# Performance work log

Measured on AMD Instinct MI355X. Metric: run time of the kernel, lower is better.

The kernel has to match this reference:

```python
import jax, jax.numpy as jnp
import numpy as np

B, T, S, E, H = 2, 2048, 2048, 1024, 16
DH = E // H

def setup_inputs() -> dict:
    key = jax.random.key(0)
    ks = jax.random.split(key, 12)
    sc = 1.0 / np.sqrt(E)
    inp = {
        'query': jax.random.normal(ks[0], (B, T, E), jnp.float32),
        'key':   jax.random.normal(ks[1], (B, S, E), jnp.float32),
        'value': jax.random.normal(ks[2], (B, S, E), jnp.float32),
        'Wq': jax.random.normal(ks[3], (E, E), jnp.float32) * sc,
        'bq': jnp.zeros((E,), jnp.float32),
        'Wk': jax.random.normal(ks[4], (E, E), jnp.float32) * sc,
        'bk': jnp.zeros((E,), jnp.float32),
        'Wv': jax.random.normal(ks[5], (E, E), jnp.float32) * sc,
        'bv': jnp.zeros((E,), jnp.float32),
        'Wo': jax.random.normal(ks[6], (E, E), jnp.float32) * sc,
        'bo': jnp.zeros((E,), jnp.float32),
    }
    return inp

def reference(query, key, value, Wq, bq, Wk, bk, Wv, bv, Wo, bo):
    # Linear projections (torch nn.Linear: x @ W.T + b)
    Q = query @ Wq.T + bq          # [B,T,E]
    K = key   @ Wk.T + bk          # [B,S,E]
    V = value @ Wv.T + bv          # [B,S,E]
    # split heads -> [B,H,L,DH]
    Q = Q.reshape(B, T, H, DH).transpose(0, 2, 1, 3)
    K = K.reshape(B, S, H, DH).transpose(0, 2, 1, 3)
    V = V.reshape(B, S, H, DH).transpose(0, 2, 1, 3)
    scores = jnp.einsum('bhtd,bhsd->bhts', Q, K) / jnp.sqrt(jnp.float32(DH))
    attn = jax.nn.softmax(scores, axis=-1)            # [B,H,T,S]
    out = jnp.einsum('bhts,bhsd->bhtd', attn, V)      # [B,H,T,DH]
    out = out.transpose(0, 2, 1, 3).reshape(B, T, E)
    out = out @ Wo.T + bo                             # [B,T,E]
    attn_avg = attn.mean(axis=1)                      # average_attn_weights=True
    return out, attn_avg
```

## Files before the change

kernel.cpp:

```cpp
#include <hip/hip_runtime.h>

#define DEV __device__ __forceinline__

typedef __attribute__((ext_vector_type(8))) short short8;
typedef __attribute__((ext_vector_type(4))) float floatx4;
typedef __attribute__((ext_vector_type(2))) unsigned int uint2v;
typedef unsigned short u16;

DEV u16 f2bf(float f) {
  unsigned int u = __float_as_uint(f);
  u += 0x7fffu + ((u >> 16) & 1u);
  return (u16)(u >> 16);
}

DEV unsigned int cvtpk(float a, float b) {
  unsigned int r;
  asm("v_cvt_pk_bf16_f32 %0, %1, %2" : "=v"(r) : "v"(a), "v"(b));
  return r;
}

DEV void load16_to_lds(const void* g, void* l) {
  __builtin_amdgcn_global_load_lds(
      (const __attribute__((address_space(1))) unsigned int*)g,
      (__attribute__((address_space(3))) unsigned int*)l, 16, 0, 0);
}

DEV int xcd_swz(int flat, int nwg) {
  return (flat & 7) * (nwg >> 3) + (flat >> 3);
}

#define MFMA16(A, B, C) __builtin_amdgcn_mfma_f32_16x16x32_bf16(A, B, C, 0, 0, 0)
#define EXP2(x) __builtin_amdgcn_exp2f(x)

#define QSCALE 0.18033688011112042f

DEV void stage_block(const u16* src_row0, int k0, int ln, void* ldsbase) {
  int r = ln >> 2;
  int p = ((ln & 3) - (ln >> 4)) & 3;
  load16_to_lds((const char*)(src_row0 + (size_t)r * 1024 + k0) + p * 16, ldsbase);
}
DEV const short8* frag_addr(const u16* base, int blk, int c, int q) {
  int slot = c * 4 + ((q + (c >> 2)) & 3);
  return (const short8*)(base + blk * 512 + slot * 8);
}

__global__ __launch_bounds__(256) void cvt_all(
    const float* __restrict__ w0, const float* __restrict__ w1,
    const float* __restrict__ w2, const float* __restrict__ w3,
    const float* __restrict__ a0, const float* __restrict__ a1, const float* __restrict__ a2,
    u16* __restrict__ e0, u16* __restrict__ e1, u16* __restrict__ e2, u16* __restrict__ e3,
    u16* __restrict__ f0, u16* __restrict__ f1, u16* __restrict__ f2) {
  const int t = blockIdx.y;
  const float* s;
  u16* d;
  size_t base;
  if (t < 4) {
    s = t == 0 ? w0 : t == 1 ? w1 : t == 2 ? w2 : w3;
    d = t == 0 ? e0 : t == 1 ? e1 : t == 2 ? e2 : e3;
    base = 0;
  } else {
    int a = (t - 4) >> 2;
    s = a == 0 ? a0 : a == 1 ? a1 : a2;
    d = a == 0 ? f0 : a == 1 ? f1 : f2;
    base = (size_t)((t - 4) & 3) * 1048576;
  }
  size_t i = base + (size_t)(blockIdx.x * 256 + threadIdx.x) * 4;
  float4 v = *(const float4*)(s + i);
  ushort4 o;
  o.x = f2bf(v.x); o.y = f2bf(v.y); o.z = f2bf(v.z); o.w = f2bf(v.w);
  *(ushort4*)(d + i) = o;
}

__global__ __launch_bounds__(512, 4) void qkv_gemm(
    const u16* __restrict__ qb, const u16* __restrict__ kb, const u16* __restrict__ vb,
    const u16* __restrict__ wq, const u16* __restrict__ wk, const u16* __restrict__ wv,
    const float* __restrict__ bq, const float* __restrict__ bk, const float* __restrict__ bv,
    u16* __restrict__ Qh, u16* __restrict__ Kh, u16* __restrict__ VT) {
  __shared__ __align__(16) u16 As[2][8192];
  __shared__ __align__(16) u16 Bs[2][4096];
  const int tid = threadIdx.x;
  const int w = tid >> 6, ln = tid & 63, q = ln >> 4, c = ln & 15;
  const int wr = w >> 1, wc = w & 1;
  const int z = blockIdx.z;
  int m_idx, n_idx;
  if (z == 2) {
    int f2 = blockIdx.x + 8 * blockIdx.y;
    n_idx = f2 & 31;
    m_idx = f2 >> 5;
  } else {
    n_idx = blockIdx.x;
    m_idx = blockIdx.y;
  }
  const int m0 = m_idx * 256, n0 = n_idx * 128;
  const u16* Asrc = z == 0 ? qb : (z == 1 ? kb : wv);
  const u16* Bsrc = z == 0 ? wq : (z == 1 ? wk : vb);

  floatx4 acc[4][4];
#pragma unroll
  for (int i = 0; i < 4; ++i)
#pragma unroll
    for (int j = 0; j < 4; ++j) acc[i][j] = (floatx4){0.f, 0.f, 0.f, 0.f};

#pragma unroll
  for (int j = 0; j < 3; ++j) {
    int idx = w * 3 + j;
    if (idx < 16)
      stage_block(Asrc + (size_t)(m0 + idx * 16) * 1024, 0, ln, (char*)As[0] + idx * 1024);
    else
      stage_block(Bsrc + (size_t)(n0 + (idx - 16) * 16) * 1024, 0, ln, (char*)Bs[0] + (idx - 16) * 1024);
  }

  int cur = 0;
  for (int k0 = 0; k0 < 1024; k0 += 32) {
    __syncthreads();
    if (k0 + 32 < 1024) {
      const int nb = cur ^ 1;
#pragma unroll
      for (int j = 0; j < 3; ++j) {
        int idx = w * 3 + j;
        if (idx < 16)
          stage_block(Asrc + (size_t)(m0 + idx * 16) * 1024, k0 + 32, ln, (char*)As[nb] + idx * 1024);
        else
          stage_block(Bsrc + (size_t)(n0 + (idx - 16) * 16) * 1024, k0 + 32, ln,
                      (char*)Bs[nb] + (idx - 16) * 1024);
      }
    }
    short8 a[4], bb[4];
#pragma unroll
    for (int mt = 0; mt < 4; ++mt) a[mt] = *frag_addr(As[cur], wr * 4 + mt, c, q);
#pragma unroll
    for (int nt = 0; nt < 4; ++nt) bb[nt] = *frag_addr(Bs[cur], wc * 4 + nt, c, q);
    __builtin_amdgcn_s_setprio(1);
#pragma unroll
    for (int mt = 0; mt < 4; ++mt)
#pragma unroll
      for (int nt = 0; nt < 4; ++nt) acc[mt][nt] = MFMA16(a[mt], bb[nt], acc[mt][nt]);
    __builtin_amdgcn_s_setprio(0);
    cur ^= 1;
  }

  if (z <= 1) {
    const float* bias = z ? bk : bq;
    u16* dst = z ? Kh : Qh;
    const float scale = z ? 1.0f : QSCALE;
    float bn[4];
#pragma unroll
    for (int nt = 0; nt < 4; ++nt) bn[nt] = bias[n0 + wc * 64 + nt * 16 + c];
#pragma unroll
    for (int mt = 0; mt < 4; ++mt)
#pragma unroll
      for (int r = 0; r < 4; ++r) {
        int m = m0 + wr * 64 + mt * 16 + 4 * q + r;
        int bbv = m >> 11, t = m & 2047;
#pragma unroll
        for (int nt = 0; nt < 4; ++nt) {
          int n = n0 + wc * 64 + nt * 16 + c;
          dst[((size_t)(bbv * 16 + (n >> 6)) * 2048 + t) * 64 + (n & 63)] =
              f2bf((acc[mt][nt][r] + bn[nt]) * scale);
        }
      }
  } else {
    float bm[4][4];
#pragma unroll
    for (int mt = 0; mt < 4; ++mt)
#pragma unroll
      for (int r = 0; r < 4; ++r) bm[mt][r] = bv[m0 + wr * 64 + mt * 16 + 4 * q + r];
#pragma unroll
    for (int mt = 0; mt < 4; ++mt)
#pragma unroll
      for (int r = 0; r < 4; ++r) {
        int d = m0 + wr * 64 + mt * 16 + 4 * q + r;
        int hh = d >> 6, dl = d & 63;
#pragma unroll
        for (int nt = 0; nt < 4; ++nt) {
          int s = n0 + wc * 64 + nt * 16 + c;
          int bbv = s >> 11, sl = s & 2047;
          VT[((size_t)(bbv * 16 + hh) * 64 + dl) * 2048 + sl] = f2bf(acc[mt][nt][r] + bm[mt][r]);
        }
      }
  }
}

__global__ __launch_bounds__(512, 4) void oproj_gemm(const u16* __restrict__ Ap, const u16* __restrict__ Wp,
                                                     const float* __restrict__ bias, float* __restrict__ out) {
  __shared__ __align__(16) u16 As[2][8192];
  __shared__ __align__(16) u16 Bs[2][4096];
  const int tid = threadIdx.x;
  const int w = tid >> 6, ln = tid & 63, q = ln >> 4, c = ln & 15;
  const int wr = w >> 1, wc = w & 1;
  const int n0 = blockIdx.x * 128, m0 = blockIdx.y * 256;

  floatx4 acc[4][4];
#pragma unroll
  for (int i = 0; i < 4; ++i)
#pragma unroll
    for (int j = 0; j < 4; ++j) acc[i][j] = (floatx4){0.f, 0.f, 0.f, 0.f};

#pragma unroll
  for (int j = 0; j < 3; ++j) {
    int idx = w * 3 + j;
    if (idx < 16)
      stage_block(Ap + (size_t)(m0 + idx * 16) * 1024, 0, ln, (char*)As[0] + idx * 1024);
    else
      stage_block(Wp + (size_t)(n0 + (idx - 16) * 16) * 1024, 0, ln, (char*)Bs[0] + (idx - 16) * 1024);
  }

  int cur = 0;
  for (int k0 = 0; k0 < 1024; k0 += 32) {
    __syncthreads();
    if (k0 + 32 < 1024) {
      const int nb = cur ^ 1;
#pragma unroll
      for (int j = 0; j < 3; ++j) {
        int idx = w * 3 + j;
        if (idx < 16)
          stage_block(Ap + (size_t)(m0 + idx * 16) * 1024, k0 + 32, ln, (char*)As[nb] + idx * 1024);
        else
          stage_block(Wp + (size_t)(n0 + (idx - 16) * 16) * 1024, k0 + 32, ln,
                      (char*)Bs[nb] + (idx - 16) * 1024);
      }
    }
    short8 a[4], bb[4];
#pragma unroll
    for (int mt = 0; mt < 4; ++mt) a[mt] = *frag_addr(As[cur], wr * 4 + mt, c, q);
#pragma unroll
    for (int nt = 0; nt < 4; ++nt) bb[nt] = *frag_addr(Bs[cur], wc * 4 + nt, c, q);
    __builtin_amdgcn_s_setprio(1);
#pragma unroll
    for (int mt = 0; mt < 4; ++mt)
#pragma unroll
      for (int nt = 0; nt < 4; ++nt) acc[mt][nt] = MFMA16(a[mt], bb[nt], acc[mt][nt]);
    __builtin_amdgcn_s_setprio(0);
    cur ^= 1;
  }

  float bn[4];
#pragma unroll
  for (int nt = 0; nt < 4; ++nt) bn[nt] = bias[n0 + wc * 64 + nt * 16 + c];
#pragma unroll
  for (int mt = 0; mt < 4; ++mt)
#pragma unroll
    for (int r = 0; r < 4; ++r) {
      int m = m0 + wr * 64 + mt * 16 + 4 * q + r;
#pragma unroll
      for (int nt = 0; nt < 4; ++nt)
        out[(size_t)m * 1024 + n0 + wc * 64 + nt * 16 + c] = acc[mt][nt][r] + bn[nt];
    }
}

__global__ __launch_bounds__(512, 4) void flash_attn(const u16* __restrict__ Qh, const u16* __restrict__ Kh,
                                                     const u16* __restrict__ VhT, u16* __restrict__ Obuf,
                                                     float* __restrict__ l_ws) {
  __shared__ __align__(16) u16 Ks[2][4096];
  __shared__ __align__(16) u16 VTs[2][4096];
  __shared__ __align__(16) u16 Ps[8][1152];
  const int tid = threadIdx.x;
  const int w = tid >> 6, ln = tid & 63, q = ln >> 4, c = ln & 15;
  const int lg = xcd_swz(blockIdx.x + 16 * (blockIdx.y + 16 * blockIdx.z), 512);
  const int t0 = (lg & 15) * 128, h = (lg >> 4) & 15, b = lg >> 8;
  const size_t bh = (size_t)(b * 16 + h);
  const u16* Qbase = Qh + bh * 131072;
  const u16* Kbase = Kh + bh * 131072;
  const u16* Vbase = VhT + bh * 131072;

  short8 qf0, qf1;
  {
    const u16* qr = Qbase + (size_t)(t0 + w * 16 + c) * 64 + q * 8;
    qf0 = *(const short8*)qr;
    qf1 = *(const short8*)(qr + 32);
  }
  floatx4 oacc[4];
  float lacc = 0.f;
#pragma unroll
  for (int j = 0; j < 4; ++j) oacc[j] = (floatx4){0.f, 0.f, 0.f, 0.f};

  const int srow = ln >> 3;
  const int sch = (ln & 7) ^ srow;
  const int cx = c & 7;
  const int row = w * 8 + srow;

  load16_to_lds((const char*)Kbase + ((size_t)row * 64 + sch * 8) * 2, (char*)Ks[0] + w * 1024);
  load16_to_lds((const char*)Vbase + ((size_t)row * 2048 + sch * 8) * 2, (char*)VTs[0] + w * 1024);

  int cur = 0;
  for (int s0 = 0; s0 < 2048; s0 += 64) {
    __syncthreads();
    if (s0 + 64 < 2048) {
      const int nb = cur ^ 1;
      load16_to_lds((const char*)Kbase + ((size_t)(s0 + 64 + row) * 64 + sch * 8) * 2,
                    (char*)Ks[nb] + w * 1024);
      load16_to_lds((const char*)Vbase + ((size_t)row * 2048 + (s0 + 64) + sch * 8) * 2,
                    (char*)VTs[nb] + w * 1024);
    }
    const u16* ks = Ks[cur];
    const u16* vs = VTs[cur];
#pragma unroll
    for (int st = 0; st < 4; ++st) {
      const int rr = st * 16 + c;
      short8 k0 = *(const short8*)(ks + rr * 64 + ((q ^ cx) << 3));
      short8 k1 = *(const short8*)(ks + rr * 64 + (((4 + q) ^ cx) << 3));
      floatx4 zz = (floatx4){0.f, 0.f, 0.f, 0.f};
      __builtin_amdgcn_s_setprio(1);
      zz = MFMA16(k0, qf0, zz);
      zz = MFMA16(k1, qf1, zz);
      __builtin_amdgcn_s_setprio(0);
      float e0 = EXP2(zz[0]), e1 = EXP2(zz[1]), e2 = EXP2(zz[2]), e3 = EXP2(zz[3]);
      lacc += (e0 + e1) + (e2 + e3);
      uint2v pk = {cvtpk(e0, e1), cvtpk(e2, e3)};
      *(uint2v*)(&Ps[w][c * 72 + st * 16 + 4 * q]) = pk;
    }
    short8 pf0 = *(const short8*)(&Ps[w][c * 72 + q * 8]);
    short8 pf1 = *(const short8*)(&Ps[w][c * 72 + 32 + q * 8]);
    __builtin_amdgcn_s_setprio(1);
#pragma unroll
    for (int dt = 0; dt < 4; ++dt) {
      const int rr = dt * 16 + c;
      short8 v0 = *(const short8*)(vs + rr * 64 + ((q ^ cx) << 3));
      short8 v1 = *(const short8*)(vs + rr * 64 + (((4 + q) ^ cx) << 3));
      oacc[dt] = MFMA16(pf0, v0, oacc[dt]);
      oacc[dt] = MFMA16(pf1, v1, oacc[dt]);
    }
    __builtin_amdgcn_s_setprio(0);
    cur ^= 1;
  }
  {
    float v = lacc;
    v += __shfl_xor(v, 16);
    v += __shfl_xor(v, 32);
    lacc = v;
    if (q == 0) l_ws[bh * 2048 + t0 + w * 16 + c] = v;
  }
#pragma unroll
  for (int r = 0; r < 4; ++r) {
    float lv = __shfl(lacc, 4 * q + r);
    float inv = __builtin_amdgcn_rcpf(lv);
    const int t = t0 + w * 16 + 4 * q + r;
#pragma unroll
    for (int dt = 0; dt < 4; ++dt)
      Obuf[((size_t)b * 2048 + t) * 1024 + h * 64 + dt * 16 + c] = f2bf(oacc[dt][r] * inv);
  }
}

__global__ __launch_bounds__(256) void attn_avg_k(const u16* __restrict__ Qh, const u16* __restrict__ Kh,
                                                  const float* __restrict__ l_ws, float* __restrict__ out2) {
  __shared__ __align__(16) u16 Ks[2][4096];
  const int tid = threadIdx.x;
  const int w = tid >> 6, ln = tid & 63, q = ln >> 4, c = ln & 15;
  const int lg = xcd_swz(blockIdx.x + 32 * (blockIdx.y + 16 * blockIdx.z), 1024);
  const int s0 = (lg & 31) * 64, t0 = ((lg >> 5) & 15) * 128, b = lg >> 9;
  const int srow = ln >> 3;
  const int sch = (ln & 7) ^ srow;
  const int cx = c & 7;

  floatx4 acc[2][4];
#pragma unroll
  for (int i = 0; i < 2; ++i)
#pragma unroll
    for (int j = 0; j < 4; ++j) acc[i][j] = (floatx4){0.f, 0.f, 0.f, 0.f};

#pragma unroll
  for (int it = 0; it < 2; ++it) {
    int I = w * 2 + it;
    int row = I * 8 + srow;
    load16_to_lds((const char*)(Kh + (size_t)(b * 16) * 131072) + ((size_t)(s0 + row) * 64 + sch * 8) * 2,
                  (char*)Ks[0] + I * 1024);
  }

  for (int h = 0; h < 16; ++h) {
    const size_t bh = (size_t)(b * 16 + h);
    const u16* ks = Ks[h & 1];
    __syncthreads();
    if (h < 15) {
      const u16* Kn = Kh + (bh + 1) * 131072;
#pragma unroll
      for (int it = 0; it < 2; ++it) {
        int I = w * 2 + it;
        int row = I * 8 + srow;
        load16_to_lds((const char*)Kn + ((size_t)(s0 + row) * 64 + sch * 8) * 2,
                      (char*)Ks[(h + 1) & 1] + I * 1024);
      }
    }
    short8 qf[2][2];
    float linv[2];
#pragma unroll
    for (int blk = 0; blk < 2; ++blk) {
      const u16* qr = Qh + bh * 131072 + (size_t)(t0 + w * 32 + blk * 16 + c) * 64 + q * 8;
      qf[blk][0] = *(const short8*)qr;
      qf[blk][1] = *(const short8*)(qr + 32);
      linv[blk] = __builtin_amdgcn_rcpf(l_ws[bh * 2048 + t0 + w * 32 + blk * 16 + c]) * 0.0625f;
    }
#pragma unroll
    for (int st = 0; st < 4; ++st) {
      const int row = st * 16 + c;
      short8 k0 = *(const short8*)(ks + row * 64 + ((q ^ cx) << 3));
      short8 k1 = *(const short8*)(ks + row * 64 + (((4 + q) ^ cx) << 3));
#pragma unroll
      for (int blk = 0; blk < 2; ++blk) {
        floatx4 zz = (floatx4){0.f, 0.f, 0.f, 0.f};
        zz = MFMA16(k0, qf[blk][0], zz);
        zz = MFMA16(k1, qf[blk][1], zz);
#pragma unroll
        for (int r = 0; r < 4; ++r) acc[blk][st][r] += EXP2(zz[r]) * linv[blk];
      }
    }
  }
#pragma unroll
  for (int blk = 0; blk < 2; ++blk) {
    const size_t t = (size_t)t0 + w * 32 + blk * 16 + c;
#pragma unroll
    for (int st = 0; st < 4; ++st) {
      float4 o;
      o.x = acc[blk][st][0]; o.y = acc[blk][st][1]; o.z = acc[blk][st][2]; o.w = acc[blk][st][3];
      *(float4*)(out2 + ((size_t)b * 2048 + t) * 2048 + s0 + st * 16 + 4 * q) = o;
    }
  }
}

extern "C" void kernel_launch(void* const* d_in, const int* in_sizes, int n_in,
                              void* d_out, int out_size, void* d_ws, size_t ws_size,
                              hipStream_t stream) {
  const float* query = (const float*)d_in[0];
  const float* key = (const float*)d_in[1];
  const float* value = (const float*)d_in[2];
  const float* Wq = (const float*)d_in[3];
  const float* bq = (const float*)d_in[4];
  const float* Wk = (const float*)d_in[5];
  const float* bk = (const float*)d_in[6];
  const float* Wv = (const float*)d_in[7];
  const float* bv = (const float*)d_in[8];
  const float* Wo = (const float*)d_in[9];
  const float* bo = (const float*)d_in[10];

  char* ws = (char*)d_ws;
  const size_t MB = 1024 * 1024;
  u16* wWq = (u16*)(ws + 0 * MB);
  u16* wWk = (u16*)(ws + 2 * MB);
  u16* wWv = (u16*)(ws + 4 * MB);
  u16* wWo = (u16*)(ws + 6 * MB);
  u16* wQh = (u16*)(ws + 8 * MB);
  u16* wKh = (u16*)(ws + 16 * MB);
  u16* wVT = (u16*)(ws + 24 * MB);
  u16* wO = (u16*)(ws + 32 * MB);
  float* wl = (float*)(ws + 40 * MB);
  float* out = (float*)d_out;
  float* out2 = out + (size_t)4194304;

  u16* qb = (u16*)out2;
  u16* kb = qb + 4194304;
  u16* vb = kb + 4194304;

  cvt_all<<<dim3(1024, 16), 256, 0, stream>>>(Wq, Wk, Wv, Wo, query, key, value,
                                              wWq, wWk, wWv, wWo, qb, kb, vb);
  qkv_gemm<<<dim3(8, 16, 3), 512, 0, stream>>>(qb, kb, vb, wWq, wWk, wWv,
                                               bq, bk, bv, wQh, wKh, wVT);
  flash_attn<<<dim3(16, 16, 2), 512, 0, stream>>>(wQh, wKh, wVT, wO, wl);
  attn_avg_k<<<dim3(32, 16, 2), 256, 0, stream>>>(wQh, wKh, wl, out2);
  oproj_gemm<<<dim3(8, 16), 512, 0, stream>>>(wO, wWo, bo, out);
}
```

Measured before the change: 280.3 us.

## Software-pipeline flash attention PV stage and shrink oproj tile to 128x128

The flash attention loop is restructured so that the QK^T MFMAs for tile i are issued before the PV MFMAs for tile i-1. V tiles are triple-buffered and P is double-buffered per wave, so the exp/softmax work can overlap with matrix-core work. A final epilogue handles the last PV step. Separately, the output projection GEMM moves to 256-thread blocks with 128x128 tiles and twice as many blocks, trading per-block reuse for more parallelism. The larger LDS footprint may reduce occupancy in the attention kernel.

```diff
diff --git a/kernel.cpp b/kernel.cpp
--- a/kernel.cpp
+++ b/kernel.cpp
@@ -181,14 +181,14 @@
   }
 }
 
-__global__ __launch_bounds__(512, 4) void oproj_gemm(const u16* __restrict__ Ap, const u16* __restrict__ Wp,
-                                                     const float* __restrict__ bias, float* __restrict__ out) {
-  __shared__ __align__(16) u16 As[2][8192];
+__global__ __launch_bounds__(256) void oproj_gemm(const u16* __restrict__ Ap, const u16* __restrict__ Wp,
+                                                  const float* __restrict__ bias, float* __restrict__ out) {
+  __shared__ __align__(16) u16 As[2][4096];
   __shared__ __align__(16) u16 Bs[2][4096];
   const int tid = threadIdx.x;
   const int w = tid >> 6, ln = tid & 63, q = ln >> 4, c = ln & 15;
   const int wr = w >> 1, wc = w & 1;
-  const int n0 = blockIdx.x * 128, m0 = blockIdx.y * 256;
+  const int n0 = blockIdx.x * 128, m0 = blockIdx.y * 128;
 
   floatx4 acc[4][4];
 #pragma unroll
@@ -197,12 +197,10 @@
     for (int j = 0; j < 4; ++j) acc[i][j] = (floatx4){0.f, 0.f, 0.f, 0.f};
 
 #pragma unroll
-  for (int j = 0; j < 3; ++j) {
-    int idx = w * 3 + j;
-    if (idx < 16)
-      stage_block(Ap + (size_t)(m0 + idx * 16) * 1024, 0, ln, (char*)As[0] + idx * 1024);
-    else
-      stage_block(Wp + (size_t)(n0 + (idx - 16) * 16) * 1024, 0, ln, (char*)Bs[0] + (idx - 16) * 1024);
+  for (int it = 0; it < 2; ++it) {
+    int I = w * 2 + it;
+    stage_block(Ap + (size_t)(m0 + I * 16) * 1024, 0, ln, (char*)As[0] + I * 1024);
+    stage_block(Wp + (size_t)(n0 + I * 16) * 1024, 0, ln, (char*)Bs[0] + I * 1024);
   }
 
   int cur = 0;
@@ -211,13 +209,10 @@
     if (k0 + 32 < 1024) {
       const int nb = cur ^ 1;
 #pragma unroll
-      for (int j = 0; j < 3; ++j) {
-        int idx = w * 3 + j;
-        if (idx < 16)
-          stage_block(Ap + (size_t)(m0 + idx * 16) * 1024, k0 + 32, ln, (char*)As[nb] + idx * 1024);
-        else
-          stage_block(Wp + (size_t)(n0 + (idx - 16) * 16) * 1024, k0 + 32, ln,
-                      (char*)Bs[nb] + (idx - 16) * 1024);
+      for (int it = 0; it < 2; ++it) {
+        int I = w * 2 + it;
+        stage_block(Ap + (size_t)(m0 + I * 16) * 1024, k0 + 32, ln, (char*)As[nb] + I * 1024);
+        stage_block(Wp + (size_t)(n0 + I * 16) * 1024, k0 + 32, ln, (char*)Bs[nb] + I * 1024);
       }
     }
     short8 a[4], bb[4];
@@ -252,8 +247,8 @@
                                                      const u16* __restrict__ VhT, u16* __restrict__ Obuf,
                                                      float* __restrict__ l_ws) {
   __shared__ __align__(16) u16 Ks[2][4096];
-  __shared__ __align__(16) u16 VTs[2][4096];
-  __shared__ __align__(16) u16 Ps[8][1152];
+  __shared__ __align__(16) u16 VTs[3][4096];
+  __shared__ __align__(16) u16 Ps[8][2][1152];
   const int tid = threadIdx.x;
   const int w = tid >> 6, ln = tid & 63, q = ln >> 4, c = ln & 15;
   const int lg = xcd_swz(blockIdx.x + 16 * (blockIdx.y + 16 * blockIdx.z), 512);
@@ -282,36 +277,64 @@
   load16_to_lds((const char*)Kbase + ((size_t)row * 64 + sch * 8) * 2, (char*)Ks[0] + w * 1024);
   load16_to_lds((const char*)Vbase + ((size_t)row * 2048 + sch * 8) * 2, (char*)VTs[0] + w * 1024);
 
-  int cur = 0;
-  for (int s0 = 0; s0 < 2048; s0 += 64) {
+  int vc = 0;
+  for (int i = 0; i < 32; ++i) {
+    const int s0 = i * 64;
     __syncthreads();
-    if (s0 + 64 < 2048) {
-      const int nb = cur ^ 1;
+    int vn = vc + 1;
+    if (vn == 3) vn = 0;
+    int vp = vc - 1;
+    if (vp < 0) vp = 2;
+    if (i + 1 < 32) {
       load16_to_lds((const char*)Kbase + ((size_t)(s0 + 64 + row) * 64 + sch * 8) * 2,
-                    (char*)Ks[nb] + w * 1024);
+                    (char*)Ks[(i + 1) & 1] + w * 1024);
       load16_to_lds((const char*)Vbase + ((size_t)row * 2048 + (s0 + 64) + sch * 8) * 2,
-                    (char*)VTs[nb] + w * 1024);
-    }
-    const u16* ks = Ks[cur];
-    const u16* vs = VTs[cur];
+                    (char*)VTs[vn] + w * 1024);
+    }
+    const u16* ks = Ks[i & 1];
+    floatx4 zz[4];
+    __builtin_amdgcn_s_setprio(1);
 #pragma unroll
     for (int st = 0; st < 4; ++st) {
       const int rr = st * 16 + c;
       short8 k0 = *(const short8*)(ks + rr * 64 + ((q ^ cx) << 3));
       short8 k1 = *(const short8*)(ks + rr * 64 + (((4 + q) ^ cx) << 3));
-      floatx4 zz = (floatx4){0.f, 0.f, 0.f, 0.f};
+      zz[st] = (floatx4){0.f, 0.f, 0.f, 0.f};
+      zz[st] = MFMA16(k0, qf0, zz[st]);
+      zz[st] = MFMA16(k1, qf1, zz[st]);
+    }
+    __builtin_amdgcn_s_setprio(0);
+    if (i > 0) {
+      const u16* vs = VTs[vp];
+      const u16* pw = Ps[w][(i - 1) & 1];
+      short8 pf0 = *(const short8*)(pw + c * 72 + q * 8);
+      short8 pf1 = *(const short8*)(pw + c * 72 + 32 + q * 8);
       __builtin_amdgcn_s_setprio(1);
-      zz = MFMA16(k0, qf0, zz);
-      zz = MFMA16(k1, qf1, zz);
+#pragma unroll
+      for (int dt = 0; dt < 4; ++dt) {
+        const int rr = dt * 16 + c;
+        short8 v0 = *(const short8*)(vs + rr * 64 + ((q ^ cx) << 3));
+        short8 v1 = *(const short8*)(vs + rr * 64 + (((4 + q) ^ cx) << 3));
+        oacc[dt] = MFMA16(pf0, v0, oacc[dt]);
+        oacc[dt] = MFMA16(pf1, v1, oacc[dt]);
+      }
       __builtin_amdgcn_s_setprio(0);
-      float e0 = EXP2(zz[0]), e1 = EXP2(zz[1]), e2 = EXP2(zz[2]), e3 = EXP2(zz[3]);
+    }
+    u16* pwr = Ps[w][i & 1];
+#pragma unroll
+    for (int st = 0; st < 4; ++st) {
+      float e0 = EXP2(zz[st][0]), e1 = EXP2(zz[st][1]), e2 = EXP2(zz[st][2]), e3 = EXP2(zz[st][3]);
       lacc += (e0 + e1) + (e2 + e3);
       uint2v pk = {cvtpk(e0, e1), cvtpk(e2, e3)};
-      *(uint2v*)(&Ps[w][c * 72 + st * 16 + 4 * q]) = pk;
-    }
-    short8 pf0 = *(const short8*)(&Ps[w][c * 72 + q * 8]);
-    short8 pf1 = *(const short8*)(&Ps[w][c * 72 + 32 + q * 8]);
-    __builtin_amdgcn_s_setprio(1);
+      *(uint2v*)(pwr + c * 72 + st * 16 + 4 * q) = pk;
+    }
+    vc = vn;
+  }
+  {
+    const u16* vs = VTs[1];
+    const u16* pw = Ps[w][1];
+    short8 pf0 = *(const short8*)(pw + c * 72 + q * 8);
+    short8 pf1 = *(const short8*)(pw + c * 72 + 32 + q * 8);
 #pragma unroll
     for (int dt = 0; dt < 4; ++dt) {
       const int rr = dt * 16 + c;
@@ -320,8 +343,6 @@
       oacc[dt] = MFMA16(pf0, v0, oacc[dt]);
       oacc[dt] = MFMA16(pf1, v1, oacc[dt]);
     }
-    __builtin_amdgcn_s_setprio(0);
-    cur ^= 1;
   }
   {
     float v = lacc;
@@ -455,5 +476,5 @@
                                                bq, bk, bv, wQh, wKh, wVT);
   flash_attn<<<dim3(16, 16, 2), 512, 0, stream>>>(wQh, wKh, wVT, wO, wl);
   attn_avg_k<<<dim3(32, 16, 2), 256, 0, stream>>>(wQh, wKh, wl, out2);
-  oproj_gemm<<<dim3(8, 16), 512, 0, stream>>>(wO, wWo, bo, out);
-}
+  oproj_gemm<<<dim3(8, 32), 256, 0, stream>>>(wO, wWo, bo, out);
+}
```

Measured after the change: 266.7 us, median of 2. 4.8% less time.
